# Performance work log

Measured on AMD Instinct MI355X. Metric: run time of the kernel, lower is better.

The kernel has to match this reference:

```python
import jax, jax.numpy as jnp
import numpy as np

GROUPS = 8
EPS = 1e-5
ALPHA = 0.2  # LeakyReLU slope
NEG = -9e15


def groupnorm(x, g, b):
    # x: [B, C, T, V]
    B, C, T, V = x.shape
    xr = x.reshape(B, GROUPS, C // GROUPS, T, V)
    mu = xr.mean(axis=(2, 3, 4), keepdims=True)
    var = xr.var(axis=(2, 3, 4), keepdims=True)
    xn = ((xr - mu) / jnp.sqrt(var + EPS)).reshape(B, C, T, V)
    return xn * g[None, :, None, None] + b[None, :, None, None]


def conv_t(x, w, bias):
    # temporal conv, kernel (k,1), 'same' padding along T
    pad = (w.shape[2] - 1) // 2
    y = jax.lax.conv_general_dilated(x, w, (1, 1), ((pad, pad), (0, 0)),
                                     dimension_numbers=('NCHW', 'OIHW', 'NCHW'))
    return y + bias[None, :, None, None]


def tcn(x, g1, b1, w, bb, g2, b2):
    h = jax.nn.relu(groupnorm(x, g1, b1))
    return groupnorm(conv_t(h, w, bb), g2, b2)  # dropout is identity in eval


def gat_heads(h, adj, w_gat, a_gat):
    # h: [BT, V, C_in]; w_gat: [H, C_in, D]; a_gat: [H, 2D, 1]
    D = w_gat.shape[-1]
    Wh = jnp.einsum('bnc,hcd->bhnd', h, w_gat)          # [BT, H, V, D]
    a1 = a_gat[:, :D, 0]                                 # [H, D]
    a2 = a_gat[:, D:, 0]                                 # [H, D]
    e1 = jnp.einsum('bhnd,hd->bhn', Wh, a1)
    e2 = jnp.einsum('bhnd,hd->bhn', Wh, a2)
    e = e1[..., :, None] + e2[..., None, :]              # [BT, H, V, V]
    e = jnp.where(e > 0, e, ALPHA * e)                   # LeakyReLU
    att = jax.nn.softmax(jnp.where(adj[None, None] > 0, e, NEG), axis=-1)
    hp = jax.nn.elu(jnp.einsum('bhnm,bhmd->bhnd', att, Wh))
    BT, H, V, _ = hp.shape
    return hp.transpose(0, 2, 1, 3).reshape(BT, V, H * D)  # concat heads


def _forward(x, adj, w_gat, a_gat,
             t3g1, t3b1, t3w, t3bb, t3g2, t3b2,
             t5g1, t5b1, t5w, t5bb, t5g2, t5b2,
             t7g1, t7b1, t7w, t7bb, t7g2, t7b2,
             fus_w, fus_b, res_w, res_b, norm_g, norm_b):
    B, C, T, V = x.shape
    h = x.transpose(0, 2, 3, 1).reshape(B * T, V, C)
    g = gat_heads(h, adj, w_gat, a_gat)                  # [B*T, V, C_out]
    C_out = g.shape[-1]
    xg = g.reshape(B, T, V, C_out).transpose(0, 3, 1, 2)  # [B, C_out, T, V]
    b3 = tcn(xg, t3g1, t3b1, t3w, t3bb, t3g2, t3b2)
    b5 = tcn(xg, t5g1, t5b1, t5w, t5bb, t5g2, t5b2)
    b7 = tcn(xg, t7g1, t7b1, t7w, t7bb, t7g2, t7b2)
    out = conv_t(jnp.concatenate([b3, b5, b7], axis=1), fus_w, fus_b)
    res = conv_t(x, res_w, res_b)                        # 1x1 residual projection
    return groupnorm(jax.nn.relu(out + res), norm_g, norm_b)


def setup_inputs() -> dict:
    key = jax.random.key(0)
    ks = jax.random.split(key, 32)
    B, C_in, T, V = 32, 64, 256, 25
    C_out, H = 128, 4
    D = C_out // H
    s = 0.1
    inp = {
        'x': jax.random.normal(ks[0], (B, C_in, T, V), jnp.float32),
        'adj': jnp.ones((V, V), jnp.float32),
        'w_gat': jax.random.normal(ks[1], (H, C_in, D), jnp.float32) * s,
        'a_gat': jax.random.normal(ks[2], (H, 2 * D, 1), jnp.float32) * s,
        'fus_w': jax.random.normal(ks[3], (C_out, 3 * C_out, 1, 1), jnp.float32) * s,
        'fus_b': jnp.zeros((C_out,), jnp.float32),
        'res_w': jax.random.normal(ks[4], (C_out, C_in, 1, 1), jnp.float32) * s,
        'res_b': jnp.zeros((C_out,), jnp.float32),
        'norm_g': jnp.ones((C_out,), jnp.float32),
        'norm_b': jnp.zeros((C_out,), jnp.float32),
    }
    for i, k in zip([3, 5, 7], [ks[5], ks[6], ks[7]]):
        inp[f't{i}g1'] = jnp.ones((C_out,), jnp.float32)
        inp[f't{i}b1'] = jnp.zeros((C_out,), jnp.float32)
        inp[f't{i}w'] = jax.random.normal(k, (C_out, C_out, i, 1), jnp.float32) * s
        inp[f't{i}bb'] = jnp.zeros((C_out,), jnp.float32)
        inp[f't{i}g2'] = jnp.ones((C_out,), jnp.float32)
        inp[f't{i}b2'] = jnp.zeros((C_out,), jnp.float32)
    return inp


def reference(x, adj, w_gat, a_gat,
              t3g1, t3b1, t3w, t3bb, t3g2, t3b2,
              t5g1, t5b1, t5w, t5bb, t5g2, t5b2,
              t7g1, t7b1, t7w, t7bb, t7g2, t7b2,
              fus_w, fus_b, res_w, res_b, norm_g, norm_b):
    return _forward(x, adj, w_gat, a_gat,
                    t3g1, t3b1, t3w, t3bb, t3g2, t3b2,
                    t5g1, t5b1, t5w, t5bb, t5g2, t5b2,
                    t7g1, t7b1, t7w, t7bb, t7g2, t7b2,
                    fus_w, fus_b, res_w, res_b, norm_g, norm_b)
```

## Files before the change

kernel.cpp:

```cpp
#include <hip/hip_runtime.h>
#include <math.h>

typedef __bf16 bf16;
typedef __bf16 bf16x8 __attribute__((ext_vector_type(8)));
typedef float  f32x4  __attribute__((ext_vector_type(4)));

constexpr int B_   = 32;
constexpr int T_   = 256;
constexpr int V_   = 25;
constexpr int NTV  = T_ * V_;
constexpr long long TENSOR = (long long)B_ * 128 * NTV;

constexpr long long ACC_OFF  = 0;
constexpr long long XGT_OFF  = 0;
constexpr long long WRB3_OFF = XGT_OFF + TENSOR / 2;
constexpr long long WRB5_OFF = WRB3_OFF + 128 * 128 * 3 / 2;
constexpr long long WRB7_OFF = WRB5_OFF + 128 * 128 * 5 / 2;
constexpr long long WGB_OFF  = WRB7_OFF + 128 * 128 * 7 / 2;
constexpr long long Y0_OFF   = ACC_OFF + TENSOR;
constexpr long long Y1_OFF   = Y0_OFF + TENSOR / 2;
constexpr long long Y2_OFF   = Y1_OFF + TENSOR / 2;
constexpr long long XT_OFF   = Y2_OFF + TENSOR / 2;
constexpr long long ABIG_OFF = XT_OFF + TENSOR / 4;
constexpr long long BIAS_OFF = ABIG_OFF + (32LL * 128 * 448) / 2;
constexpr long long STATS_OFF = BIAS_OFF + 4096;
constexpr long long P1_OFF = STATS_OFF + 2560;
constexpr long long P2_OFF = P1_OFF + 32LL * 256 * 16;
constexpr long long P3_OFF = P2_OFF + 3LL * 32 * 50 * 16;

__device__ __forceinline__ float bflo(unsigned u) { return __builtin_bit_cast(float, u << 16); }
__device__ __forceinline__ float bfhi(unsigned u) { return __builtin_bit_cast(float, u & 0xffff0000u); }
__device__ __forceinline__ unsigned packbf2(float a, float b) {
    unsigned short ua = __builtin_bit_cast(unsigned short, (bf16)a);
    unsigned short ub = __builtin_bit_cast(unsigned short, (bf16)b);
    return (unsigned)ua | ((unsigned)ub << 16);
}

__global__ void repack_wbf16_kernel(const float* __restrict__ w, bf16* __restrict__ wr, int K) {
    int idx = blockIdx.x * 256 + threadIdx.x;
    int tot = 128 * 128 * K;
    if (idx >= tot) return;
    int e    = idx & 7;
    int lane = (idx >> 3) & 63;
    int rem  = idx >> 9;
    int cb   = rem & 3;
    int rem2 = rem >> 2;
    int dt   = rem2 % K;
    int cb_co = rem2 / K;
    int l15 = lane & 15, l4 = lane >> 4;
    int co = cb_co * 16 + l15;
    int ci = cb * 32 + l4 * 8 + e;
    wr[idx] = (bf16)w[(co * 128 + ci) * K + dt];
}

__global__ void repack_wgbl_kernel(const float* __restrict__ wg, bf16* __restrict__ wgbl) {
    int idx = blockIdx.x * 256 + threadIdx.x;
    if (idx >= 8192) return;
    int e = idx & 7;
    int lane = (idx >> 3) & 63;
    int q = idx >> 9;
    int cb_co = q >> 1, cb = q & 1;
    int co = cb_co * 16 + (lane & 15);
    int ci = cb * 32 + (lane >> 4) * 8 + e;
    int h = co >> 5, d = co & 31;
    wgbl[idx] = (bf16)wg[h * 2048 + ci * 32 + d];
}

__global__ __launch_bounds__(256) void reduce_stats_kernel(const float* __restrict__ pbuf, int ntiles,
                                                           float* __restrict__ st,
                                                           long long pstride, int sstride) {
    __shared__ float s_v[256];
    int b = blockIdx.x, seg = blockIdx.y, t = threadIdx.x;
    const float* p = pbuf + (long long)seg * pstride + ((long long)b * ntiles) * 16;
    int slot = t & 15;
    int chunk = t >> 4;
    float acc = 0.f;
    for (int i = chunk; i < ntiles; i += 16)
        acc += p[i * 16 + slot];
    s_v[t] = acc;
    __syncthreads();
    for (int off = 8; off > 0; off >>= 1) {
        if (chunk < off) s_v[t] += s_v[t + off * 16];
        __syncthreads();
    }
    if (t < 8) {
        float s = s_v[t], q = s_v[t + 8];
        float mu = s * (1.f / 102400.f);
        float var = q * (1.f / 102400.f) - mu * mu;
        float* so = st + (long long)seg * sstride;
        so[b * 8 + t] = mu;
        so[256 + b * 8 + t] = rsqrtf(var + 1e-5f);
    }
}

__global__ __launch_bounds__(256) void gat_fused_kernel(const float* __restrict__ x,
                                                        const bf16* __restrict__ wgbl,
                                                        const float* __restrict__ adj,
                                                        const float* __restrict__ ag,
                                                        bf16* __restrict__ xgt,
                                                        bf16* __restrict__ xt,
                                                        float* __restrict__ p1) {
    __shared__ __align__(16) bf16 s_xt[32 * 64];
    __shared__ float s_wh[25 * 132];
    __shared__ float s_att[100 * 28];
    __shared__ float s_e1[100], s_e2[100];
    __shared__ float s_adj[625];
    __shared__ float s_rs[256], s_rq[256];

    int tile = blockIdx.x, b = blockIdx.y, tid = threadIdx.x;
    long long nb0 = (long long)b * NTV + tile * 25;

    {
        int r = tid >> 3, ch = tid & 7;
        uint4 o = {0u, 0u, 0u, 0u};
        if (r < 25) {
            const float* xp = x + ((long long)(b * 64 + ch * 8)) * NTV + tile * 25 + r;
            float v[8];
#pragma unroll
            for (int e = 0; e < 8; ++e) v[e] = xp[(long long)e * NTV];
            o.x = packbf2(v[0], v[1]);
            o.y = packbf2(v[2], v[3]);
            o.z = packbf2(v[4], v[5]);
            o.w = packbf2(v[6], v[7]);
        }
        *reinterpret_cast<uint4*>(s_xt + r * 64 + ((ch ^ (r & 7)) << 3)) = o;
    }
    for (int o = tid; o < 625; o += 256) s_adj[o] = adj[o];
    __syncthreads();

    if (tid < 200) {
        int r = tid >> 3, ch = tid & 7;
        uint4 v = *reinterpret_cast<const uint4*>(s_xt + r * 64 + (ch ^ (r & 7)) * 8);
        *reinterpret_cast<uint4*>(xt + (nb0 + r) * 64 + ch * 8) = v;
    }

    int wid = tid >> 6, lane = tid & 63, l15 = lane & 15, l4 = lane >> 4;
    int co0 = wid * 32;

    f32x4 acc[2][2];
#pragma unroll
    for (int m = 0; m < 2; ++m)
#pragma unroll
        for (int ns = 0; ns < 2; ++ns) acc[m][ns] = f32x4{0.f, 0.f, 0.f, 0.f};
#pragma unroll
    for (int cb = 0; cb < 2; ++cb) {
        bf16x8 a0 = *(const bf16x8*)(wgbl + (((wid * 2 + 0) * 2 + cb) * 64 + lane) * 8);
        bf16x8 a1 = *(const bf16x8*)(wgbl + (((wid * 2 + 1) * 2 + cb) * 64 + lane) * 8);
#pragma unroll
        for (int ns = 0; ns < 2; ++ns) {
            int r = ns * 16 + l15;
            int chunk = (cb * 4 + l4) ^ (r & 7);
            bf16x8 bv = *(const bf16x8*)(s_xt + r * 64 + chunk * 8);
            acc[0][ns] = __builtin_amdgcn_mfma_f32_16x16x32_bf16(a0, bv, acc[0][ns], 0, 0, 0);
            acc[1][ns] = __builtin_amdgcn_mfma_f32_16x16x32_bf16(a1, bv, acc[1][ns], 0, 0, 0);
        }
    }

    float4 a1v[2], a2v[2];
#pragma unroll
    for (int m = 0; m < 2; ++m) {
        a1v[m] = *reinterpret_cast<const float4*>(ag + wid * 64 + m * 16 + l4 * 4);
        a2v[m] = *reinterpret_cast<const float4*>(ag + wid * 64 + 32 + m * 16 + l4 * 4);
    }
#pragma unroll
    for (int ns = 0; ns < 2; ++ns) {
        int r = ns * 16 + l15;
        if (r < 25) {
            *reinterpret_cast<float4*>(&s_wh[r * 132 + co0 + l4 * 4]) =
                float4{acc[0][ns][0], acc[0][ns][1], acc[0][ns][2], acc[0][ns][3]};
            *reinterpret_cast<float4*>(&s_wh[r * 132 + co0 + 16 + l4 * 4]) =
                float4{acc[1][ns][0], acc[1][ns][1], acc[1][ns][2], acc[1][ns][3]};
        }
        float pe1 = acc[0][ns][0] * a1v[0].x + acc[0][ns][1] * a1v[0].y
                  + acc[0][ns][2] * a1v[0].z + acc[0][ns][3] * a1v[0].w
                  + acc[1][ns][0] * a1v[1].x + acc[1][ns][1] * a1v[1].y
                  + acc[1][ns][2] * a1v[1].z + acc[1][ns][3] * a1v[1].w;
        float pe2 = acc[0][ns][0] * a2v[0].x + acc[0][ns][1] * a2v[0].y
                  + acc[0][ns][2] * a2v[0].z + acc[0][ns][3] * a2v[0].w
                  + acc[1][ns][0] * a2v[1].x + acc[1][ns][1] * a2v[1].y
                  + acc[1][ns][2] * a2v[1].z + acc[1][ns][3] * a2v[1].w;
        pe1 += __shfl_xor(pe1, 16); pe1 += __shfl_xor(pe1, 32);
        pe2 += __shfl_xor(pe2, 16); pe2 += __shfl_xor(pe2, 32);
        if (l4 == 0 && r < 25) { s_e1[r * 4 + wid] = pe1; s_e2[r * 4 + wid] = pe2; }
    }
    __syncthreads();

    if (tid < 100) {
        int h = tid / 25, i = tid - h * 25;
        float ei = s_e1[i * 4 + h];
        float ev[25];
        float mx = -3.4e38f;
#pragma unroll
        for (int j = 0; j < 25; j++) {
            float e = ei + s_e2[j * 4 + h];
            e = e > 0.f ? e : 0.2f * e;
            e = (s_adj[i * 25 + j] > 0.f) ? e : -9.0e15f;
            ev[j] = e;
            mx = fmaxf(mx, e);
        }
        float sum = 0.f;
#pragma unroll
        for (int j = 0; j < 25; j++) { float p = __expf(ev[j] - mx); ev[j] = p; sum += p; }
        float inv = 1.f / sum;
        int row = (h * 25 + i) * 28;
#pragma unroll
        for (int j = 0; j < 25; j++) s_att[row + j] = ev[j] * inv;
        s_att[row + 25] = 0.f; s_att[row + 26] = 0.f; s_att[row + 27] = 0.f;
    }
    __syncthreads();

    int hd = tid & 127, vh = tid >> 7;
    int v0 = vh * 13, nv = vh ? 12 : 13;
    int h = hd >> 5;
    float whr[28];
#pragma unroll
    for (int j = 0; j < 25; ++j) whr[j] = s_wh[j * 132 + hd];
    whr[25] = 0.f; whr[26] = 0.f; whr[27] = 0.f;
    float accp[13];
#pragma unroll
    for (int i = 0; i < 13; i++) accp[i] = 0.f;
#pragma unroll
    for (int i = 0; i < 13; i++) {
        int row = (h * 25 + v0 + i) * 28;
#pragma unroll
        for (int j4 = 0; j4 < 7; ++j4) {
            float4 a4 = *reinterpret_cast<const float4*>(&s_att[row + j4 * 4]);
            accp[i] += a4.x * whr[j4 * 4] + a4.y * whr[j4 * 4 + 1]
                     + a4.z * whr[j4 * 4 + 2] + a4.w * whr[j4 * 4 + 3];
        }
    }

    float ssum = 0.f, qsum = 0.f;
    for (int i = 0; i < nv; i++) {
        float val = accp[i];
        val = val > 0.f ? val : expm1f(val);
        bf16 bv = (bf16)val;
        xgt[(nb0 + v0 + i) * 128 + hd] = bv;
        float f = (float)bv;
        ssum += f; qsum += f * f;
    }
    s_rs[tid] = ssum; s_rq[tid] = qsum;
    __syncthreads();
    if (tid < 8) {
        float ss = 0.f, qq = 0.f;
#pragma unroll
        for (int k = 0; k < 16; ++k) {
            int ch = tid * 16 + k;
            ss += s_rs[ch] + s_rs[ch + 128];
            qq += s_rq[ch] + s_rq[ch + 128];
        }
        float* pp = p1 + ((long long)(b * 256 + tile)) * 16;
        pp[tid] = ss;
        pp[8 + tid] = qq;
    }
}

template <int K>
__global__ __launch_bounds__(256) void conv_mfma_kernel(const bf16* __restrict__ xgt,
                                                        const bf16* __restrict__ wr,
                                                        const float* __restrict__ bb,
                                                        const float* __restrict__ g1,
                                                        const float* __restrict__ b1,
                                                        const float* __restrict__ stats1,
                                                        bf16* __restrict__ y,
                                                        float* __restrict__ p2) {
    constexpr int P = (K - 1) / 2;
    constexpr int ROWS = 128 + (K - 1) * 25;
    constexpr int NCH = ROWS * 16;
    constexpr int ITERS = (NCH + 255) / 256;
    __shared__ bf16 s_h[ROWS * 128];
    __shared__ float s_sc[128], s_bc[128];
    __shared__ float s_ps[8], s_pq[8];

    int tile = blockIdx.x, b = blockIdx.y, tid = threadIdx.x;
    int n0 = tile * 128;
    if (tid < 128) {
        int g = tid >> 4;
        float mu = stats1[b * 8 + g], rs = stats1[256 + b * 8 + g];
        float sc = rs * g1[tid];
        s_sc[tid] = sc;
        s_bc[tid] = b1[tid] - mu * sc;
    }
    __syncthreads();

    int ch = tid & 15;
    float sc8[8], bc8[8];
#pragma unroll
    for (int j = 0; j < 8; ++j) { sc8[j] = s_sc[ch * 8 + j]; bc8[j] = s_bc[ch * 8 + j]; }

    int nb = b * NTV;
    for (int it = 0; it < ITERS; ++it) {
        int flat = it * 256 + tid;
        if (flat < NCH) {
            int r = flat >> 4;
            int n = n0 - P * 25 + r;
            uint4 v = {0u, 0u, 0u, 0u};
            if ((unsigned)n < (unsigned)NTV)
                v = *reinterpret_cast<const uint4*>(xgt + ((long long)(nb + n)) * 128 + ch * 8);
            unsigned w[4] = {v.x, v.y, v.z, v.w};
            uint4 o;
            unsigned* op = &o.x;
#pragma unroll
            for (int p = 0; p < 4; ++p) {
                float f0 = fmaxf(bflo(w[p]) * sc8[2 * p] + bc8[2 * p], 0.f);
                float f1 = fmaxf(bfhi(w[p]) * sc8[2 * p + 1] + bc8[2 * p + 1], 0.f);
                op[p] = packbf2(f0, f1);
            }
            *reinterpret_cast<uint4*>(s_h + r * 128 + (ch ^ (r & 15)) * 8) = o;
        }
    }
    __syncthreads();

    int wid = tid >> 6, lane = tid & 63, l15 = lane & 15, l4 = lane >> 4;
    int co0 = wid * 32;
    f32x4 acc[2][8];
#pragma unroll
    for (int m = 0; m < 2; ++m)
#pragma unroll
        for (int ns = 0; ns < 8; ++ns) acc[m][ns] = f32x4{0.f, 0.f, 0.f, 0.f};

    const bf16* wrA = wr + lane * 8;
    for (int dt = 0; dt < K; ++dt) {
#pragma unroll
        for (int cb = 0; cb < 4; ++cb) {
            bf16x8 a0 = *(const bf16x8*)(wrA + (((wid * 2 + 0) * K + dt) * 4 + cb) * 512);
            bf16x8 a1 = *(const bf16x8*)(wrA + (((wid * 2 + 1) * K + dt) * 4 + cb) * 512);
#pragma unroll
            for (int ns = 0; ns < 8; ++ns) {
                int r = ns * 16 + l15 + dt * 25;
                int chunk = (cb * 4 + l4) ^ (r & 15);
                bf16x8 bv = *(const bf16x8*)(s_h + r * 128 + chunk * 8);
                acc[0][ns] = __builtin_amdgcn_mfma_f32_16x16x32_bf16(a0, bv, acc[0][ns], 0, 0, 0);
                acc[1][ns] = __builtin_amdgcn_mfma_f32_16x16x32_bf16(a1, bv, acc[1][ns], 0, 0, 0);
            }
        }
    }
    __syncthreads();

    bf16* sy = s_h;
    float bias[2][4];
#pragma unroll
    for (int m = 0; m < 2; ++m)
#pragma unroll
        for (int rr = 0; rr < 4; ++rr) bias[m][rr] = bb[co0 + m * 16 + l4 * 4 + rr];
    float ssum[2] = {0.f, 0.f}, qsum[2] = {0.f, 0.f};
#pragma unroll
    for (int m = 0; m < 2; ++m)
#pragma unroll
        for (int ns = 0; ns < 8; ++ns) {
            int nl = ns * 16 + l15;
            uint2 pk;
            pk.x = packbf2(acc[m][ns][0] + bias[m][0], acc[m][ns][1] + bias[m][1]);
            pk.y = packbf2(acc[m][ns][2] + bias[m][2], acc[m][ns][3] + bias[m][3]);
            float f0 = bflo(pk.x), f1 = bfhi(pk.x), f2 = bflo(pk.y), f3 = bfhi(pk.y);
            ssum[m] += f0 + f1 + f2 + f3;
            qsum[m] += f0 * f0 + f1 * f1 + f2 * f2 + f3 * f3;
            *reinterpret_cast<uint2*>(sy + nl * 136 + co0 + m * 16 + l4 * 4) = pk;
        }
#pragma unroll
    for (int m = 0; m < 2; ++m) {
        float s = ssum[m], q = qsum[m];
#pragma unroll
        for (int off = 32; off > 0; off >>= 1) { s += __shfl_xor(s, off); q += __shfl_xor(q, off); }
        if (lane == 0) { s_ps[wid * 2 + m] = s; s_pq[wid * 2 + m] = q; }
    }
    __syncthreads();
    if (tid < 8) {
        float* pp = p2 + ((long long)(b * 50 + tile)) * 16;
        pp[tid] = s_ps[tid];
        pp[8 + tid] = s_pq[tid];
    }
#pragma unroll
    for (int it = 0; it < 8; ++it) {
        int flat = it * 256 + tid;
        int nl = flat >> 4, c2 = flat & 15;
        uint4 v = *reinterpret_cast<const uint4*>(sy + nl * 136 + c2 * 8);
        *reinterpret_cast<uint4*>(y + ((long long)(nb + n0 + nl)) * 128 + c2 * 8) = v;
    }
}

__global__ __launch_bounds__(256) void fold_kernel(const float* __restrict__ fus_w, const float* __restrict__ fus_b,
                                                   const float* __restrict__ res_w, const float* __restrict__ res_b,
                                                   const float* __restrict__ g20, const float* __restrict__ b20,
                                                   const float* __restrict__ g21, const float* __restrict__ b21,
                                                   const float* __restrict__ g22, const float* __restrict__ b22,
                                                   const float* __restrict__ st0, const float* __restrict__ st1,
                                                   const float* __restrict__ st2,
                                                   bf16* __restrict__ Abig, float* __restrict__ biasb) {
    __shared__ float s_sc[384], s_bc[384];
    int b = blockIdx.x, cb_co = blockIdx.y, tid = threadIdx.x;
    int co0 = cb_co * 16;
    for (int o = tid; o < 384; o += 256) {
        int k = o >> 7, cc = o & 127, g = cc >> 4;
        const float* st = (k == 0) ? st0 : (k == 1) ? st1 : st2;
        const float* gg = (k == 0) ? g20 : (k == 1) ? g21 : g22;
        const float* b2 = (k == 0) ? b20 : (k == 1) ? b21 : b22;
        float mu = st[b * 8 + g], rs = st[256 + b * 8 + g];
        float sc = rs * gg[cc];
        s_sc[o] = sc;
        s_bc[o] = b2[cc] - mu * sc;
    }
    __syncthreads();

    bf16* abase = Abig + ((long long)(b * 8 + cb_co)) * 14 * 512;
#pragma unroll 1
    for (int it = 0; it < 28; ++it) {
        int o = it * 256 + tid;
        int e = o & 7;
        int lane = (o >> 3) & 63;
        int ks = o >> 9;
        int l15 = lane & 15, l4 = lane >> 4;
        int co = co0 + l15;
        int j = ks * 32 + l4 * 8 + e;
        float val = (j < 384) ? fus_w[co * 384 + j] * s_sc[j] : res_w[co * 64 + (j - 384)];
        abase[o] = (bf16)val;
    }

    int co_l = tid >> 4, part = tid & 15;
    int co = co0 + co_l;
    float s = 0.f;
#pragma unroll
    for (int k = 0; k < 24; ++k) {
        int j = part + k * 16;
        s += fus_w[co * 384 + j] * s_bc[j];
    }
#pragma unroll
    for (int off = 1; off < 16; off <<= 1) s += __shfl_xor(s, off);
    if (part == 0)
        biasb[b * 128 + co] = fus_b[co] + res_b[co] + s;
}

__global__ __launch_bounds__(256) void fuse_mfma_kernel(const bf16* __restrict__ y0, const bf16* __restrict__ y1,
                                                        const bf16* __restrict__ y2, const bf16* __restrict__ xt,
                                                        const bf16* __restrict__ Abig, const float* __restrict__ biasb,
                                                        float* __restrict__ accf, float* __restrict__ p3) {
    __shared__ __align__(16) bf16 s_b[32 * 448];
    __shared__ float s_ps[8], s_pq[8];
    int tile = blockIdx.x, b = blockIdx.y, tid = threadIdx.x;
    int n0 = tile * 32;

    int c = tid % 56;
    int roff = tid / 56;
    bool act = tid < 224;
    const bf16* src;
    int stride;
    if (c < 48) {
        src = (c < 16 ? y0 : (c < 32 ? y1 : y2)) + (c & 15) * 8;
        stride = 128;
    } else {
        src = xt + (c - 48) * 8;
        stride = 64;
    }
    src += (long long)(b * NTV + n0) * stride;
    if (act) {
#pragma unroll
        for (int it = 0; it < 8; ++it) {
            int r = it * 4 + roff;
            uint4 v = *reinterpret_cast<const uint4*>(src + (long long)r * stride);
            *reinterpret_cast<uint4*>(s_b + r * 448 + (c ^ (r & 7)) * 8) = v;
        }
    }
    __syncthreads();

    int wid = tid >> 6, lane = tid & 63, l15 = lane & 15, l4 = lane >> 4;
    int co0 = wid * 32;
    f32x4 acc[2][2];
#pragma unroll
    for (int m = 0; m < 2; ++m)
#pragma unroll
        for (int ns = 0; ns < 2; ++ns) acc[m][ns] = f32x4{0.f, 0.f, 0.f, 0.f};

    const bf16* abase = Abig + (((long long)(b * 8 + wid * 2)) * 14 * 64 + lane) * 8;
#pragma unroll
    for (int ks = 0; ks < 14; ++ks) {
        bf16x8 a0 = *(const bf16x8*)(abase + ks * 512);
        bf16x8 a1 = *(const bf16x8*)(abase + 14 * 512 + ks * 512);
        int ci = ks * 4 + l4;
#pragma unroll
        for (int ns = 0; ns < 2; ++ns) {
            int r = ns * 16 + l15;
            bf16x8 bv = *(const bf16x8*)(s_b + r * 448 + (ci ^ (r & 7)) * 8);
            acc[0][ns] = __builtin_amdgcn_mfma_f32_16x16x32_bf16(a0, bv, acc[0][ns], 0, 0, 0);
            acc[1][ns] = __builtin_amdgcn_mfma_f32_16x16x32_bf16(a1, bv, acc[1][ns], 0, 0, 0);
        }
    }

    float bias[2][4];
#pragma unroll
    for (int m = 0; m < 2; ++m)
#pragma unroll
        for (int rr = 0; rr < 4; ++rr) bias[m][rr] = biasb[b * 128 + co0 + m * 16 + l4 * 4 + rr];

    __syncthreads();
    float* s_yf = reinterpret_cast<float*>(s_b);
    float ssum[2] = {0.f, 0.f}, qsum[2] = {0.f, 0.f};
#pragma unroll
    for (int m = 0; m < 2; ++m)
#pragma unroll
        for (int ns = 0; ns < 2; ++ns) {
            int nl = ns * 16 + l15;
            float4 val;
            val.x = acc[m][ns][0] + bias[m][0];
            val.y = acc[m][ns][1] + bias[m][1];
            val.z = acc[m][ns][2] + bias[m][2];
            val.w = acc[m][ns][3] + bias[m][3];
            float r0 = fmaxf(val.x, 0.f), r1 = fmaxf(val.y, 0.f);
            float r2 = fmaxf(val.z, 0.f), r3 = fmaxf(val.w, 0.f);
            ssum[m] += r0 + r1 + r2 + r3;
            qsum[m] += r0 * r0 + r1 * r1 + r2 * r2 + r3 * r3;
            *reinterpret_cast<float4*>(s_yf + nl * 136 + co0 + m * 16 + l4 * 4) = val;
        }
#pragma unroll
    for (int m = 0; m < 2; ++m) {
        float s = ssum[m], q = qsum[m];
#pragma unroll
        for (int off = 32; off > 0; off >>= 1) { s += __shfl_xor(s, off); q += __shfl_xor(q, off); }
        if (lane == 0) { s_ps[wid * 2 + m] = s; s_pq[wid * 2 + m] = q; }
    }
    __syncthreads();
    if (tid < 8) {
        float* pp = p3 + ((long long)(b * 200 + tile)) * 16;
        pp[tid] = s_ps[tid];
        pp[8 + tid] = s_pq[tid];
    }
#pragma unroll
    for (int it = 0; it < 4; ++it) {
        int flat = it * 256 + tid;
        int nl = flat >> 5, cq = flat & 31;
        float4 v = *reinterpret_cast<const float4*>(s_yf + nl * 136 + cq * 4);
        *reinterpret_cast<float4*>(accf + ((long long)(b * NTV + n0 + nl)) * 128 + cq * 4) = v;
    }
}

__global__ __launch_bounds__(256) void final_kernel(const float* __restrict__ accf,
                                                    const float* __restrict__ stats3,
                                                    const float* __restrict__ ng,
                                                    const float* __restrict__ nb,
                                                    float* __restrict__ out) {
    __shared__ float s_o[128 * 72];
    __shared__ float s_sc[128], s_bc[128];
    int tile = blockIdx.x, b = blockIdx.y, tid = threadIdx.x;
    int n0 = tile * 64;
    if (tid < 128) {
        int g = tid >> 4;
        float mu = stats3[b * 8 + g], rs = stats3[256 + b * 8 + g];
        float sv = rs * ng[tid];
        s_sc[tid] = sv;
        s_bc[tid] = nb[tid] - mu * sv;
    }
    __syncthreads();
#pragma unroll
    for (int it = 0; it < 8; ++it) {
        int flat = it * 256 + tid;
        int r = flat >> 5, cq = flat & 31;
        float4 v = *reinterpret_cast<const float4*>(accf + ((long long)(b * NTV + n0 + r)) * 128 + cq * 4);
        float f[4] = {v.x, v.y, v.z, v.w};
#pragma unroll
        for (int p = 0; p < 4; ++p) {
            int ci = cq * 4 + p;
            s_o[ci * 72 + r] = fmaxf(f[p], 0.f) * s_sc[ci] + s_bc[ci];
        }
    }
    __syncthreads();
#pragma unroll
    for (int it = 0; it < 8; ++it) {
        int flat = it * 256 + tid;
        int ci = flat >> 4, q = flat & 15;
        float4 v = *reinterpret_cast<const float4*>(s_o + ci * 72 + q * 4);
        *reinterpret_cast<float4*>(out + ((long long)(b * 128 + ci)) * NTV + n0 + q * 4) = v;
    }
}

extern "C" void kernel_launch(void* const* d_in, const int* in_sizes, int n_in,
                              void* d_out, int out_size, void* d_ws, size_t ws_size,
                              hipStream_t stream) {
    const float* x      = (const float*)d_in[0];
    const float* adj    = (const float*)d_in[1];
    const float* w_gat  = (const float*)d_in[2];
    const float* a_gat  = (const float*)d_in[3];
    const float* fus_w  = (const float*)d_in[4];
    const float* fus_b  = (const float*)d_in[5];
    const float* res_w  = (const float*)d_in[6];
    const float* res_b  = (const float*)d_in[7];
    const float* norm_g = (const float*)d_in[8];
    const float* norm_b = (const float*)d_in[9];
    const float* tg1[3], *tb1[3], *tw[3], *tbb[3], *tg2[3], *tb2[3];
    for (int i = 0; i < 3; i++) {
        tg1[i] = (const float*)d_in[10 + 6 * i + 0];
        tb1[i] = (const float*)d_in[10 + 6 * i + 1];
        tw[i]  = (const float*)d_in[10 + 6 * i + 2];
        tbb[i] = (const float*)d_in[10 + 6 * i + 3];
        tg2[i] = (const float*)d_in[10 + 6 * i + 4];
        tb2[i] = (const float*)d_in[10 + 6 * i + 5];
    }

    float* ws = (float*)d_ws;
    float* accf  = ws + ACC_OFF;
    bf16* xgt    = (bf16*)(ws + XGT_OFF);
    bf16* wrb[3] = { (bf16*)(ws + WRB3_OFF), (bf16*)(ws + WRB5_OFF), (bf16*)(ws + WRB7_OFF) };
    bf16* wgbl   = (bf16*)(ws + WGB_OFF);
    bf16* yb[3]  = { (bf16*)(ws + Y0_OFF), (bf16*)(ws + Y1_OFF), (bf16*)(ws + Y2_OFF) };
    bf16* xt     = (bf16*)(ws + XT_OFF);
    bf16* Abig   = (bf16*)(ws + ABIG_OFF);
    float* biasb = ws + BIAS_OFF;
    float* S1    = ws + STATS_OFF;
    float* S2    = S1 + 512;
    float* S3    = S1 + 2048;
    float* P1    = ws + P1_OFF;
    float* P2    = ws + P2_OFF;
    float* P3    = ws + P3_OFF;

    const int Ks[3] = { 3, 5, 7 };

    for (int i = 0; i < 3; i++) {
        int tot = 128 * 128 * Ks[i];
        repack_wbf16_kernel<<<(tot + 255) / 256, 256, 0, stream>>>(tw[i], wrb[i], Ks[i]);
    }
    repack_wgbl_kernel<<<32, 256, 0, stream>>>(w_gat, wgbl);

    dim3 g64(100, 32), g128(50, 32), g32f(200, 32), ggat(256, 32);

    gat_fused_kernel<<<ggat, 256, 0, stream>>>(x, wgbl, adj, a_gat, xgt, xt, P1);
    reduce_stats_kernel<<<dim3(32, 1), 256, 0, stream>>>(P1, 256, S1, 0, 0);

    conv_mfma_kernel<3><<<g128, 256, 0, stream>>>(xgt, wrb[0], tbb[0], tg1[0], tb1[0], S1, yb[0], P2);
    conv_mfma_kernel<5><<<g128, 256, 0, stream>>>(xgt, wrb[1], tbb[1], tg1[1], tb1[1], S1, yb[1], P2 + 25600);
    conv_mfma_kernel<7><<<g128, 256, 0, stream>>>(xgt, wrb[2], tbb[2], tg1[2], tb1[2], S1, yb[2], P2 + 51200);
    reduce_stats_kernel<<<dim3(32, 3), 256, 0, stream>>>(P2, 50, S2, 25600, 512);

    fold_kernel<<<dim3(32, 8), 256, 0, stream>>>(fus_w, fus_b, res_w, res_b,
                                                 tg2[0], tb2[0], tg2[1], tb2[1], tg2[2], tb2[2],
                                                 S2, S2 + 512, S2 + 1024, Abig, biasb);

    fuse_mfma_kernel<<<g32f, 256, 0, stream>>>(yb[0], yb[1], yb[2], xt, Abig, biasb, accf, P3);
    reduce_stats_kernel<<<dim3(32, 1), 256, 0, stream>>>(P3, 200, S3, 0, 0);

    final_kernel<<<g64, 256, 0, stream>>>(accf, S3, norm_g, norm_b, (float*)d_out);
}
```

Baseline: 445.7 us.

## Merge weight repacks and three temporal convs into single launches, fast ELU

Combines the four weight-repack kernels into one prep kernel and the three templated temporal-conv kernels into one launch that picks the kernel size from blockIdx.z. This cuts launch count and lets the three branches fill the GPU together instead of running back to back. The ELU switches from expm1f to __expf(x)-1, which loses accuracy near zero. Every block now reserves shared memory for the largest (K=7) tile, which can lower occupancy for the K=3 and K=5 blocks.

```diff
diff --git a/kernel.cpp b/kernel.cpp
--- a/kernel.cpp
+++ b/kernel.cpp
@@ -36,34 +36,38 @@
     return (unsigned)ua | ((unsigned)ub << 16);
 }
 
-__global__ void repack_wbf16_kernel(const float* __restrict__ w, bf16* __restrict__ wr, int K) {
+constexpr int N3 = 128 * 128 * 3;
+constexpr int N5 = 128 * 128 * 5;
+constexpr int N7 = 128 * 128 * 7;
+constexpr int NW = N3 + N5 + N7;
+constexpr int PREP_TOT = NW + 8192;
+
+__global__ void prep_kernel(const float* __restrict__ w3, const float* __restrict__ w5,
+                            const float* __restrict__ w7, const float* __restrict__ wg,
+                            bf16* __restrict__ wr3, bf16* __restrict__ wr5, bf16* __restrict__ wr7,
+                            bf16* __restrict__ wgbl) {
     int idx = blockIdx.x * 256 + threadIdx.x;
-    int tot = 128 * 128 * K;
-    if (idx >= tot) return;
-    int e    = idx & 7;
-    int lane = (idx >> 3) & 63;
-    int rem  = idx >> 9;
-    int cb   = rem & 3;
-    int rem2 = rem >> 2;
-    int dt   = rem2 % K;
-    int cb_co = rem2 / K;
-    int l15 = lane & 15, l4 = lane >> 4;
-    int co = cb_co * 16 + l15;
-    int ci = cb * 32 + l4 * 8 + e;
-    wr[idx] = (bf16)w[(co * 128 + ci) * K + dt];
-}
-
-__global__ void repack_wgbl_kernel(const float* __restrict__ wg, bf16* __restrict__ wgbl) {
-    int idx = blockIdx.x * 256 + threadIdx.x;
-    if (idx >= 8192) return;
-    int e = idx & 7;
-    int lane = (idx >> 3) & 63;
-    int q = idx >> 9;
-    int cb_co = q >> 1, cb = q & 1;
-    int co = cb_co * 16 + (lane & 15);
-    int ci = cb * 32 + (lane >> 4) * 8 + e;
-    int h = co >> 5, d = co & 31;
-    wgbl[idx] = (bf16)wg[h * 2048 + ci * 32 + d];
+    if (idx < NW) {
+        const float* w; bf16* wr; int K; int i = idx;
+        if (i < N3)           { w = w3; wr = wr3; K = 3; }
+        else if (i < N3 + N5) { i -= N3; w = w5; wr = wr5; K = 5; }
+        else                  { i -= N3 + N5; w = w7; wr = wr7; K = 7; }
+        int e = i & 7, lane = (i >> 3) & 63, rem = i >> 9;
+        int cb = rem & 3, rem2 = rem >> 2;
+        int dt = rem2 % K, cb_co = rem2 / K;
+        int l15 = lane & 15, l4 = lane >> 4;
+        int co = cb_co * 16 + l15;
+        int ci = cb * 32 + l4 * 8 + e;
+        wr[i] = (bf16)w[(co * 128 + ci) * K + dt];
+    } else if (idx < PREP_TOT) {
+        int i = idx - NW;
+        int e = i & 7, lane = (i >> 3) & 63, q = i >> 9;
+        int cb_co = q >> 1, cb = q & 1;
+        int co = cb_co * 16 + (lane & 15);
+        int ci = cb * 32 + (lane >> 4) * 8 + e;
+        int h = co >> 5, d = co & 31;
+        wgbl[i] = (bf16)wg[h * 2048 + ci * 32 + d];
+    }
 }
 
 __global__ __launch_bounds__(256) void reduce_stats_kernel(const float* __restrict__ pbuf, int ntiles,
@@ -233,7 +237,7 @@
     float ssum = 0.f, qsum = 0.f;
     for (int i = 0; i < nv; i++) {
         float val = accp[i];
-        val = val > 0.f ? val : expm1f(val);
+        val = val > 0.f ? val : (__expf(val) - 1.f);
         bf16 bv = (bf16)val;
         xgt[(nb0 + v0 + i) * 128 + hd] = bv;
         float f = (float)bv;
@@ -256,23 +260,23 @@
 }
 
 template <int K>
-__global__ __launch_bounds__(256) void conv_mfma_kernel(const bf16* __restrict__ xgt,
-                                                        const bf16* __restrict__ wr,
-                                                        const float* __restrict__ bb,
-                                                        const float* __restrict__ g1,
-                                                        const float* __restrict__ b1,
-                                                        const float* __restrict__ stats1,
-                                                        bf16* __restrict__ y,
-                                                        float* __restrict__ p2) {
+__device__ __forceinline__ void conv_body(bf16* __restrict__ s_h,
+                                          float* __restrict__ s_sc, float* __restrict__ s_bc,
+                                          float* __restrict__ s_ps, float* __restrict__ s_pq,
+                                          const bf16* __restrict__ xgt,
+                                          const bf16* __restrict__ wr,
+                                          const float* __restrict__ bb,
+                                          const float* __restrict__ g1,
+                                          const float* __restrict__ b1,
+                                          const float* __restrict__ stats1,
+                                          bf16* __restrict__ y,
+                                          float* __restrict__ p2,
+                                          int tile, int b, int tid) {
     constexpr int P = (K - 1) / 2;
     constexpr int ROWS = 128 + (K - 1) * 25;
     constexpr int NCH = ROWS * 16;
     constexpr int ITERS = (NCH + 255) / 256;
-    __shared__ bf16 s_h[ROWS * 128];
-    __shared__ float s_sc[128], s_bc[128];
-    __shared__ float s_ps[8], s_pq[8];
-
-    int tile = blockIdx.x, b = blockIdx.y, tid = threadIdx.x;
+
     int n0 = tile * 128;
     if (tid < 128) {
         int g = tid >> 4;
@@ -376,6 +380,44 @@
         int nl = flat >> 4, c2 = flat & 15;
         uint4 v = *reinterpret_cast<const uint4*>(sy + nl * 136 + c2 * 8);
         *reinterpret_cast<uint4*>(y + ((long long)(nb + n0 + nl)) * 128 + c2 * 8) = v;
+    }
+}
+
+__global__ __launch_bounds__(256) void conv_all_kernel(const bf16* __restrict__ xgt,
+                                                       const bf16* __restrict__ wr3,
+                                                       const bf16* __restrict__ wr5,
+                                                       const bf16* __restrict__ wr7,
+                                                       const float* __restrict__ bb3,
+                                                       const float* __restrict__ bb5,
+                                                       const float* __restrict__ bb7,
+                                                       const float* __restrict__ g13,
+                                                       const float* __restrict__ g15,
+                                                       const float* __restrict__ g17,
+                                                       const float* __restrict__ b13,
+                                                       const float* __restrict__ b15,
+                                                       const float* __restrict__ b17,
+                                                       const float* __restrict__ stats1,
+                                                       bf16* __restrict__ y0,
+                                                       bf16* __restrict__ y1,
+                                                       bf16* __restrict__ y2,
+                                                       float* __restrict__ p2) {
+    __shared__ bf16 s_h[278 * 128];
+    __shared__ float s_sc[128], s_bc[128];
+    __shared__ float s_ps[8], s_pq[8];
+    int tile = blockIdx.x, b = blockIdx.y, tid = threadIdx.x;
+    switch (blockIdx.z) {
+        case 0:
+            conv_body<3>(s_h, s_sc, s_bc, s_ps, s_pq, xgt, wr3, bb3, g13, b13,
+                         stats1, y0, p2, tile, b, tid);
+            break;
+        case 1:
+            conv_body<5>(s_h, s_sc, s_bc, s_ps, s_pq, xgt, wr5, bb5, g15, b15,
+                         stats1, y1, p2 + 25600, tile, b, tid);
+            break;
+        default:
+            conv_body<7>(s_h, s_sc, s_bc, s_ps, s_pq, xgt, wr7, bb7, g17, b17,
+                         stats1, y2, p2 + 51200, tile, b, tid);
+            break;
     }
 }
 
@@ -610,22 +652,19 @@
     float* P2    = ws + P2_OFF;
     float* P3    = ws + P3_OFF;
 
-    const int Ks[3] = { 3, 5, 7 };
-
-    for (int i = 0; i < 3; i++) {
-        int tot = 128 * 128 * Ks[i];
-        repack_wbf16_kernel<<<(tot + 255) / 256, 256, 0, stream>>>(tw[i], wrb[i], Ks[i]);
-    }
-    repack_wgbl_kernel<<<32, 256, 0, stream>>>(w_gat, wgbl);
-
-    dim3 g64(100, 32), g128(50, 32), g32f(200, 32), ggat(256, 32);
+    prep_kernel<<<(PREP_TOT + 255) / 256, 256, 0, stream>>>(tw[0], tw[1], tw[2], w_gat,
+                                                            wrb[0], wrb[1], wrb[2], wgbl);
+
+    dim3 g64(100, 32), gconv(50, 32, 3), g32f(200, 32), ggat(256, 32);
 
     gat_fused_kernel<<<ggat, 256, 0, stream>>>(x, wgbl, adj, a_gat, xgt, xt, P1);
     reduce_stats_kernel<<<dim3(32, 1), 256, 0, stream>>>(P1, 256, S1, 0, 0);
 
-    conv_mfma_kernel<3><<<g128, 256, 0, stream>>>(xgt, wrb[0], tbb[0], tg1[0], tb1[0], S1, yb[0], P2);
-    conv_mfma_kernel<5><<<g128, 256, 0, stream>>>(xgt, wrb[1], tbb[1], tg1[1], tb1[1], S1, yb[1], P2 + 25600);
-    conv_mfma_kernel<7><<<g128, 256, 0, stream>>>(xgt, wrb[2], tbb[2], tg1[2], tb1[2], S1, yb[2], P2 + 51200);
+    conv_all_kernel<<<gconv, 256, 0, stream>>>(xgt, wrb[0], wrb[1], wrb[2],
+                                               tbb[0], tbb[1], tbb[2],
+                                               tg1[0], tg1[1], tg1[2],
+                                               tb1[0], tb1[1], tb1[2],
+                                               S1, yb[0], yb[1], yb[2], P2);
     reduce_stats_kernel<<<dim3(32, 3), 256, 0, stream>>>(P2, 50, S2, 25600, 512);
 
     fold_kernel<<<dim3(32, 8), 256, 0, stream>>>(fus_w, fus_b, res_w, res_b,
```

Measured after the change: 409.1 us. 1.09x faster.
